# Kernel optimization log

Measured on AMD Instinct MI355X. Metric: run time of the kernel, lower is better.

## Reference

```python
import jax, jax.numpy as jnp
import numpy as np

TOP_K = 2
LN_EPS = 1e-6


def setup_inputs() -> dict:
    key = jax.random.key(0)
    ks = jax.random.split(key, 8)
    B, T, D, FF, E = 4, 512, 1024, 4096, 8
    x = jax.random.normal(ks[0], (B, T, D), dtype=jnp.float32)
    gate_w = jax.random.normal(ks[1], (E, D), dtype=jnp.float32) * (1.0 / np.sqrt(D))
    ln_g = jnp.ones((E, D), dtype=jnp.float32)
    ln_b = jnp.zeros((E, D), dtype=jnp.float32)
    w1 = jax.random.normal(ks[2], (E, FF, D), dtype=jnp.float32) * (1.0 / np.sqrt(D))
    b1 = jnp.zeros((E, FF), dtype=jnp.float32)
    w2 = jax.random.normal(ks[3], (E, D, FF), dtype=jnp.float32) * (1.0 / np.sqrt(FF))
    b2 = jnp.zeros((E, D), dtype=jnp.float32)
    return {"x": x, "gate_w": gate_w, "ln_g": ln_g, "ln_b": ln_b,
            "w1": w1, "b1": b1, "w2": w2, "b2": b2}


def reference(x, gate_w, ln_g, ln_b, w1, b1, w2, b2):
    B, T, D = x.shape
    E = gate_w.shape[0]
    N = B * T
    xf = x.reshape(N, D)

    # ---- Router: linear gate -> softmax -> top-k dispatch mask + aux loss ----
    logits = xf @ gate_w.T                          # [N, E]
    scores = jax.nn.softmax(logits, axis=-1)        # [N, E]
    topk_vals, topk_idx = jax.lax.top_k(scores, TOP_K)
    dispatch = jnp.zeros_like(scores).at[
        jnp.arange(N)[:, None], topk_idx].set(1.0)  # [N, E] 0/1 mask
    load = dispatch.sum(axis=0)                     # [E]
    importance = scores.sum(axis=0)                 # [E]
    aux_loss = (importance * load).sum() * E / (N * N)

    # ---- Experts (PositionwiseFeedForward, kernel_size=1, skip connection) ----
    # Dense-all-experts compute, masked combine: identical math to the
    # per-expert gather/scatter loop in the torch module.
    mu = xf.mean(axis=-1, keepdims=True)
    var = ((xf - mu) ** 2).mean(axis=-1, keepdims=True)
    norm = (xf - mu) / jnp.sqrt(var + LN_EPS)       # [N, D]
    xe = norm[:, None, :] * ln_g[None] + ln_b[None] # [N, E, D] per-expert LN
    h = jax.nn.relu(jnp.einsum('ned,efd->nef', xe, w1) + b1[None])  # [N, E, FF]
    y = jnp.einsum('nef,edf->ned', h, w2) + b2[None] + xf[:, None, :]  # +skip

    comb = scores * dispatch                        # top-k gate weights [N, E]
    out = jnp.einsum('ne,ned->nd', comb, y).reshape(B, T, D)
    return out, aux_loss
```

## Files before the change

### kernel.cpp

```cpp
#include <hip/hip_runtime.h>
#include <hip/hip_bf16.h>

#define N_TOK 2048
#define DMODEL 1024
#define NEXP 8
#define FFDIM 4096
#define NMAX 2048
#define PADROWS 5120
#define TMAX 40

#define BM 128
#define BN 128
#define BK 64
#define KSPL 4

typedef __attribute__((ext_vector_type(8))) short s16x8;
typedef __attribute__((ext_vector_type(4))) float f32x4;

__device__ __forceinline__ float bf2f(ushort u) {
    union { uint i; float f; } x; x.i = ((uint)u) << 16; return x.f;
}
__device__ __forceinline__ ushort f2bf(float f) {
    union { float f; uint i; } x; x.f = f;
    uint r = x.i + 0x7fffu + ((x.i >> 16) & 1u);
    return (ushort)(r >> 16);
}

__device__ __forceinline__ void gl_lds16(const void* g, void* l) {
    __builtin_amdgcn_global_load_lds(
        (const __attribute__((address_space(1))) unsigned int*)g,
        (__attribute__((address_space(3))) unsigned int*)l, 16, 0, 0);
}

__device__ __forceinline__ float block_sum(float v, float* s4) {
    #pragma unroll
    for (int off = 32; off; off >>= 1) v += __shfl_down(v, off);
    __syncthreads();
    if ((threadIdx.x & 63) == 0) s4[threadIdx.x >> 6] = v;
    __syncthreads();
    return s4[0] + s4[1] + s4[2] + s4[3];
}

__global__ __launch_bounds__(256)
void router_kernel(const float* __restrict__ x, const float* __restrict__ gate_w,
                   ushort* __restrict__ norm, float* __restrict__ scores,
                   int* __restrict__ cnt, int* __restrict__ lists,
                   int4* __restrict__ info, float2* __restrict__ gpair) {
    __shared__ float s4[4];
    const int n = blockIdx.x, tid = threadIdx.x;
    const float* xr = x + (size_t)n * DMODEL;
    float4 v = *(const float4*)(xr + tid * 4);

    float tot = block_sum(v.x + v.y + v.z + v.w, s4);
    float mu = tot * (1.0f / DMODEL);
    float d0 = v.x - mu, d1 = v.y - mu, d2 = v.z - mu, d3 = v.w - mu;
    float var = block_sum(d0 * d0 + d1 * d1 + d2 * d2 + d3 * d3, s4) * (1.0f / DMODEL);
    float rstd = rsqrtf(var + 1e-6f);

    ushort nb[4] = { f2bf(d0 * rstd), f2bf(d1 * rstd), f2bf(d2 * rstd), f2bf(d3 * rstd) };
    *(uint2*)(norm + (size_t)n * DMODEL + tid * 4) = *(uint2*)nb;

    float lg[NEXP];
    #pragma unroll
    for (int e = 0; e < NEXP; ++e) {
        float4 g = *(const float4*)(gate_w + (size_t)e * DMODEL + tid * 4);
        lg[e] = v.x * g.x + v.y * g.y + v.z * g.z + v.w * g.w;
    }
    #pragma unroll
    for (int e = 0; e < NEXP; ++e) lg[e] = block_sum(lg[e], s4);

    if (tid == 0) {
        float m = lg[0];
        #pragma unroll
        for (int e = 1; e < NEXP; ++e) m = fmaxf(m, lg[e]);
        float ex[NEXP], Z = 0.f;
        #pragma unroll
        for (int e = 0; e < NEXP; ++e) { ex[e] = expf(lg[e] - m); Z += ex[e]; }
        float inv = 1.0f / Z;
        float sc[NEXP];
        #pragma unroll
        for (int e = 0; e < NEXP; ++e) { sc[e] = ex[e] * inv; scores[n * NEXP + e] = sc[e]; }
        int i1 = 0;
        #pragma unroll
        for (int e = 1; e < NEXP; ++e) if (sc[e] > sc[i1]) i1 = e;
        int i2 = (i1 == 0) ? 1 : 0;
        #pragma unroll
        for (int e = 0; e < NEXP; ++e) if (e != i1 && sc[e] > sc[i2]) i2 = e;
        int s1 = atomicAdd(&cnt[i1], 1);
        lists[i1 * NMAX + s1] = n;
        int s2 = atomicAdd(&cnt[i2], 1);
        lists[i2 * NMAX + s2] = n;
        info[n] = make_int4(i1, s1, i2, s2);
        gpair[n] = make_float2(sc[i1], sc[i2]);
    }
}

__global__ __launch_bounds__(256)
void prep_kernel(const float* __restrict__ scores, const int* __restrict__ cnt,
                 int* __restrict__ offs_pad, int* __restrict__ ntiles,
                 int4* __restrict__ tilemap, float* __restrict__ aux_out) {
    __shared__ float s4[4];
    __shared__ float imp[NEXP];
    float part[NEXP] = {};
    for (int i = threadIdx.x; i < N_TOK; i += 256) {
        #pragma unroll
        for (int e = 0; e < NEXP; ++e) part[e] += scores[i * NEXP + e];
    }
    #pragma unroll
    for (int e = 0; e < NEXP; ++e) {
        float s = block_sum(part[e], s4);
        if (threadIdx.x == 0) imp[e] = s;
    }
    __syncthreads();
    if (threadIdx.x == 0) {
        float aux = 0.f; int pad = 0, idx = 0;
        #pragma unroll
        for (int e = 0; e < NEXP; ++e) {
            aux += imp[e] * (float)cnt[e];
            offs_pad[e] = pad;
            int tiles = (cnt[e] + BM - 1) / BM;
            for (int t = 0; t < tiles; ++t)
                tilemap[idx++] = make_int4(e, pad + t * BM, 0, 0);
            pad += tiles * BM;
        }
        offs_pad[NEXP] = pad;
        ntiles[0] = idx;
        aux_out[0] = aux * (float)NEXP / ((float)N_TOK * (float)N_TOK);
    }
}

__global__ __launch_bounds__(256)
void gather_kernel(const ushort* __restrict__ norm, const float* __restrict__ ln_g,
                   const float* __restrict__ ln_b, const int* __restrict__ offs_pad,
                   const int* __restrict__ cnt, const int* __restrict__ lists,
                   ushort* __restrict__ A1) {
    const int r = blockIdx.x;
    int e = 0;
    #pragma unroll
    for (int k = 1; k < NEXP; ++k) if (r >= offs_pad[k]) e = k;
    const int slot = r - offs_pad[e];
    const int t4 = threadIdx.x * 4;
    if (slot >= cnt[e]) {
        ushort z[4] = {};
        *(uint2*)(A1 + (size_t)r * DMODEL + t4) = *(uint2*)z;
        return;
    }
    const int token = lists[e * NMAX + slot];
    uint2 nbv = *(const uint2*)(norm + (size_t)token * DMODEL + t4);
    ushort ns[4]; *(uint2*)ns = nbv;
    float4 gv = *(const float4*)(ln_g + (size_t)e * DMODEL + t4);
    float4 bv = *(const float4*)(ln_b + (size_t)e * DMODEL + t4);
    ushort ob[4] = { f2bf(bf2f(ns[0]) * gv.x + bv.x), f2bf(bf2f(ns[1]) * gv.y + bv.y),
                     f2bf(bf2f(ns[2]) * gv.z + bv.z), f2bf(bf2f(ns[3]) * gv.w + bv.w) };
    *(uint2*)(A1 + (size_t)r * DMODEL + t4) = *(uint2*)ob;
}

template<int KDIM, int NT, int KSPLT, bool RELU>
__global__ __launch_bounds__(256, 3)
void moe_gemm(const ushort* __restrict__ A, const float* __restrict__ W,
              const float* __restrict__ bias, const int* __restrict__ ntiles,
              const int4* __restrict__ tilemap, ushort* __restrict__ hout,
              float* __restrict__ yout) {
    __shared__ ushort As[BM * BK];
    __shared__ float  Wsf[BN * BK];
    constexpr int NOUT = NT * BN;

    const int q = (int)gridDim.x >> 3;
    const int logical = ((int)blockIdx.x & 7) * q + ((int)blockIdx.x >> 3);
    const int bt = logical % TMAX;
    int g = logical / TMAX;
    if (bt >= ntiles[0]) return;
    const int nt = g % NT;
    const int kb = g / NT;
    const int4 tm = tilemap[bt];
    const int e = tm.x, row0 = tm.y;

    const int tid = threadIdx.x, lane = tid & 63, wave = tid >> 6;
    const int wm = (wave & 1) * 64, wn = (wave >> 1) * 64;
    const int trow = lane >> 3;
    const int scol = ((lane & 7) ^ trow) * 8;

    const ushort* Agb = A + (size_t)row0 * KDIM;
    const float*  Wgb = W + ((size_t)e * NOUT + nt * BN) * KDIM;

    const int wrow  = (lane >> 4);
    const int wchnk = (lane & 15);

    f32x4 acc[4][4] = {};

    auto stageA = [&](int step) {
        #pragma unroll
        for (int i = 0; i < 4; ++i) {
            int c = wave * 4 + i;
            gl_lds16(Agb + (size_t)(c * 8 + trow) * KDIM + step * BK + scol, &As[c * 512]);
        }
    };
    auto stageW = [&](int step) {
        #pragma unroll
        for (int i = 0; i < 8; ++i) {
            int r0 = wave * 32 + i * 4;
            int row = r0 + wrow;
            int chunk = wchnk ^ (row & 7);
            gl_lds16(Wgb + (size_t)row * KDIM + step * BK + chunk * 4, &Wsf[r0 * 64]);
        }
    };
    auto readW = [&](int ni, int kki) -> s16x8 {
        const int row = wn + ni * 16 + (lane & 15);
        const int x = row & 7;
        const int cb = kki * 8 + (lane >> 4) * 2;
        const float4 f0 = *(const float4*)&Wsf[row * 64 + ((cb ^ x) << 2)];
        const float4 f1 = *(const float4*)&Wsf[row * 64 + (((cb + 1) ^ x) << 2)];
        union { s16x8 v; __hip_bfloat162 h2[4]; } u;
        u.h2[0] = __float22bfloat162_rn(make_float2(f0.x, f0.y));
        u.h2[1] = __float22bfloat162_rn(make_float2(f0.z, f0.w));
        u.h2[2] = __float22bfloat162_rn(make_float2(f1.x, f1.y));
        u.h2[3] = __float22bfloat162_rn(make_float2(f1.z, f1.w));
        return u.v;
    };
    auto mfma_phase = [&]() {
        #pragma unroll
        for (int kki = 0; kki < 2; ++kki) {
            const int cx = (kki * 32 + (lane >> 4) * 8) ^ ((lane & 7) << 3);
            s16x8 af[4], bfv[4];
            #pragma unroll
            for (int mi = 0; mi < 4; ++mi)
                af[mi] = *(const s16x8*)&As[(wm + mi * 16 + (lane & 15)) * BK + cx];
            #pragma unroll
            for (int ni = 0; ni < 4; ++ni)
                bfv[ni] = readW(ni, kki);
            #pragma unroll
            for (int mi = 0; mi < 4; ++mi)
                #pragma unroll
                for (int ni = 0; ni < 4; ++ni)
                    acc[mi][ni] = __builtin_amdgcn_mfma_f32_16x16x32_bf16(
                        af[mi], bfv[ni], acc[mi][ni], 0, 0, 0);
        }
    };

    const int KS = KDIM / BK / KSPLT;
    const int kt0 = kb * KS;

    for (int s = 0; s < KS; ++s) {
        stageA(kt0 + s);
        stageW(kt0 + s);
        __syncthreads();
        mfma_phase();
        __syncthreads();
    }

    if (RELU) {
        #pragma unroll
        for (int ni = 0; ni < 4; ++ni) {
            const int nn = nt * BN + wn + ni * 16 + (lane & 15);
            const float bv = bias[(size_t)e * NOUT + nn];
            #pragma unroll
            for (int mi = 0; mi < 4; ++mi)
                #pragma unroll
                for (int r = 0; r < 4; ++r) {
                    const int sl = wm + mi * 16 + ((lane >> 4) << 2) + r;
                    hout[(size_t)(row0 + sl) * NOUT + nn] =
                        f2bf(fmaxf(acc[mi][ni][r] + bv, 0.f));
                }
        }
    } else {
        #pragma unroll
        for (int ni = 0; ni < 4; ++ni) {
            const int nn = nt * BN + wn + ni * 16 + (lane & 15);
            #pragma unroll
            for (int mi = 0; mi < 4; ++mi)
                #pragma unroll
                for (int r = 0; r < 4; ++r) {
                    const int sl = wm + mi * 16 + ((lane >> 4) << 2) + r;
                    yout[((size_t)kb * PADROWS + row0 + sl) * NOUT + nn] = acc[mi][ni][r];
                }
        }
    }
}

__global__ __launch_bounds__(256)
void combine_kernel(const float* __restrict__ ypart, const float* __restrict__ b2,
                    const float* __restrict__ x, const int* __restrict__ offs_pad,
                    const int4* __restrict__ info, const float2* __restrict__ gpair,
                    float* __restrict__ out) {
    const int n = blockIdx.x, d = threadIdx.x * 4;
    const int4 ii = info[n];
    const float2 g = gpair[n];
    const int r1 = offs_pad[ii.x] + ii.y, r2 = offs_pad[ii.z] + ii.w;
    f32x4 y1 = {}, y2 = {};
    #pragma unroll
    for (int kb = 0; kb < KSPL; ++kb) {
        y1 += *(const f32x4*)(ypart + ((size_t)kb * PADROWS + r1) * DMODEL + d);
        y2 += *(const f32x4*)(ypart + ((size_t)kb * PADROWS + r2) * DMODEL + d);
    }
    const f32x4 b21 = *(const f32x4*)(b2 + (size_t)ii.x * DMODEL + d);
    const f32x4 b22 = *(const f32x4*)(b2 + (size_t)ii.z * DMODEL + d);
    const f32x4 xv  = *(const f32x4*)(x + (size_t)n * DMODEL + d);
    f32x4 o = g.x * (y1 + b21 + xv) + g.y * (y2 + b22 + xv);
    *(f32x4*)(out + (size_t)n * DMODEL + d) = o;
}

extern "C" void kernel_launch(void* const* d_in, const int* in_sizes, int n_in,
                              void* d_out, int out_size, void* d_ws, size_t ws_size,
                              hipStream_t stream) {
    const float* x      = (const float*)d_in[0];
    const float* gate_w = (const float*)d_in[1];
    const float* ln_g   = (const float*)d_in[2];
    const float* ln_b   = (const float*)d_in[3];
    const float* w1     = (const float*)d_in[4];
    const float* b1     = (const float*)d_in[5];
    const float* w2     = (const float*)d_in[6];
    const float* b2     = (const float*)d_in[7];
    float* out = (float*)d_out;

    char* w = (char*)d_ws;
    int*    cnt      = (int*)(w + 0);
    int*    offs_pad = (int*)(w + 64);
    int*    ntiles   = (int*)(w + 128);
    int4*   tilemap  = (int4*)(w + 192);
    int*    lists    = (int*)(w + 1024);
    float*  scores   = (float*)(w + 66560);
    int4*   info     = (int4*)(w + 132096);
    float2* gpair    = (float2*)(w + 164864);
    ushort* norm     = (ushort*)(w + 181248);
    ushort* A1       = (ushort*)(w + 4375552);
    ushort* h        = (ushort*)(w + 14861312);
    float*  ypart    = (float*)(w + 56804352);

    hipMemsetAsync(cnt, 0, 64, stream);

    router_kernel<<<N_TOK, 256, 0, stream>>>(x, gate_w, norm, scores, cnt, lists, info, gpair);
    prep_kernel<<<1, 256, 0, stream>>>(scores, cnt, offs_pad, ntiles, tilemap,
                                       out + (size_t)N_TOK * DMODEL);
    gather_kernel<<<PADROWS, 256, 0, stream>>>(norm, ln_g, ln_b, offs_pad, cnt, lists, A1);
    moe_gemm<DMODEL, FFDIM / BN, 1, true><<<TMAX * (FFDIM / BN), 256, 0, stream>>>(
        A1, w1, b1, ntiles, tilemap, h, nullptr);
    moe_gemm<FFDIM, DMODEL / BN, KSPL, false><<<TMAX * (DMODEL / BN) * KSPL, 256, 0, stream>>>(
        h, w2, nullptr, ntiles, tilemap, nullptr, ypart);
    combine_kernel<<<N_TOK, 256, 0, stream>>>(ypart, b2, x, offs_pad, info, gpair, out);
}
```

Measured before the change: 258.3 us.

## Double-buffer GEMM tiles and convert weights to bf16 once before LDS store

The MoE GEMM now double-buffers the A and W shared-memory tiles and prefetches the next K-step while the MFMAs for the current step run, which leaves one barrier per iteration. Weights are loaded into registers as fp32, converted to bf16 once and written to LDS with an XOR swizzle. Before, fp32 was stored in LDS and every wave converted it again when reading. This halves W's LDS footprint and removes the repeated conversions, but it adds register pressure from the prefetch registers, and occupancy drops from 3 to 2 blocks per CU.

```diff
diff --git a/kernel.cpp b/kernel.cpp
--- a/kernel.cpp
+++ b/kernel.cpp
@@ -156,13 +156,13 @@
 }
 
 template<int KDIM, int NT, int KSPLT, bool RELU>
-__global__ __launch_bounds__(256, 3)
+__global__ __launch_bounds__(256, 2)
 void moe_gemm(const ushort* __restrict__ A, const float* __restrict__ W,
               const float* __restrict__ bias, const int* __restrict__ ntiles,
               const int4* __restrict__ tilemap, ushort* __restrict__ hout,
               float* __restrict__ yout) {
-    __shared__ ushort As[BM * BK];
-    __shared__ float  Wsf[BN * BK];
+    __shared__ ushort As[2][BM * BK];
+    __shared__ ushort Ws[2][BN * BK];
     constexpr int NOUT = NT * BN;
 
     const int q = (int)gridDim.x >> 3;
@@ -183,51 +183,49 @@
     const ushort* Agb = A + (size_t)row0 * KDIM;
     const float*  Wgb = W + ((size_t)e * NOUT + nt * BN) * KDIM;
 
-    const int wrow  = (lane >> 4);
-    const int wchnk = (lane & 15);
-
     f32x4 acc[4][4] = {};
-
-    auto stageA = [&](int step) {
+    float4 wr[8];
+
+    auto stageA = [&](int step, int b) {
         #pragma unroll
         for (int i = 0; i < 4; ++i) {
             int c = wave * 4 + i;
-            gl_lds16(Agb + (size_t)(c * 8 + trow) * KDIM + step * BK + scol, &As[c * 512]);
+            gl_lds16(Agb + (size_t)(c * 8 + trow) * KDIM + step * BK + scol, &As[b][c * 512]);
         }
     };
-    auto stageW = [&](int step) {
-        #pragma unroll
-        for (int i = 0; i < 8; ++i) {
-            int r0 = wave * 32 + i * 4;
-            int row = r0 + wrow;
-            int chunk = wchnk ^ (row & 7);
-            gl_lds16(Wgb + (size_t)row * KDIM + step * BK + chunk * 4, &Wsf[r0 * 64]);
+    auto loadWreg = [&](int step) {
+        #pragma unroll
+        for (int i = 0; i < 4; ++i) {
+            int c = tid + 256 * i;
+            const float* p = Wgb + (size_t)(c >> 3) * KDIM + step * BK + (c & 7) * 8;
+            wr[2 * i]     = *(const float4*)p;
+            wr[2 * i + 1] = *(const float4*)(p + 4);
         }
     };
-    auto readW = [&](int ni, int kki) -> s16x8 {
-        const int row = wn + ni * 16 + (lane & 15);
-        const int x = row & 7;
-        const int cb = kki * 8 + (lane >> 4) * 2;
-        const float4 f0 = *(const float4*)&Wsf[row * 64 + ((cb ^ x) << 2)];
-        const float4 f1 = *(const float4*)&Wsf[row * 64 + (((cb + 1) ^ x) << 2)];
-        union { s16x8 v; __hip_bfloat162 h2[4]; } u;
-        u.h2[0] = __float22bfloat162_rn(make_float2(f0.x, f0.y));
-        u.h2[1] = __float22bfloat162_rn(make_float2(f0.z, f0.w));
-        u.h2[2] = __float22bfloat162_rn(make_float2(f1.x, f1.y));
-        u.h2[3] = __float22bfloat162_rn(make_float2(f1.z, f1.w));
-        return u.v;
+    auto cvtWriteW = [&](int b) {
+        #pragma unroll
+        for (int i = 0; i < 4; ++i) {
+            int c = tid + 256 * i;
+            int row = c >> 3, col8 = (c & 7) * 8;
+            union { s16x8 v; __hip_bfloat162 h2[4]; } u;
+            u.h2[0] = __float22bfloat162_rn(make_float2(wr[2 * i].x, wr[2 * i].y));
+            u.h2[1] = __float22bfloat162_rn(make_float2(wr[2 * i].z, wr[2 * i].w));
+            u.h2[2] = __float22bfloat162_rn(make_float2(wr[2 * i + 1].x, wr[2 * i + 1].y));
+            u.h2[3] = __float22bfloat162_rn(make_float2(wr[2 * i + 1].z, wr[2 * i + 1].w));
+            *(s16x8*)&Ws[b][row * BK + (col8 ^ ((row & 7) << 3))] = u.v;
+        }
     };
-    auto mfma_phase = [&]() {
+    auto mfma_phase = [&](int b) {
         #pragma unroll
         for (int kki = 0; kki < 2; ++kki) {
             const int cx = (kki * 32 + (lane >> 4) * 8) ^ ((lane & 7) << 3);
             s16x8 af[4], bfv[4];
             #pragma unroll
             for (int mi = 0; mi < 4; ++mi)
-                af[mi] = *(const s16x8*)&As[(wm + mi * 16 + (lane & 15)) * BK + cx];
+                af[mi] = *(const s16x8*)&As[b][(wm + mi * 16 + (lane & 15)) * BK + cx];
             #pragma unroll
             for (int ni = 0; ni < 4; ++ni)
-                bfv[ni] = readW(ni, kki);
+                bfv[ni] = *(const s16x8*)&Ws[b][(wn + ni * 16 + (lane & 15)) * BK + cx];
             #pragma unroll
             for (int mi = 0; mi < 4; ++mi)
                 #pragma unroll
@@ -240,12 +238,21 @@
     const int KS = KDIM / BK / KSPLT;
     const int kt0 = kb * KS;
 
+    loadWreg(kt0);
+    stageA(kt0, 0);
+    cvtWriteW(0);
+    __syncthreads();
+
+    int buf = 0;
     for (int s = 0; s < KS; ++s) {
-        stageA(kt0 + s);
-        stageW(kt0 + s);
+        if (s + 1 < KS) {
+            stageA(kt0 + s + 1, buf ^ 1);
+            loadWreg(kt0 + s + 1);
+        }
+        mfma_phase(buf);
+        if (s + 1 < KS) cvtWriteW(buf ^ 1);
         __syncthreads();
-        mfma_phase();
-        __syncthreads();
+        buf ^= 1;
     }
 
     if (RELU) {
```

Measured after the change: 309.9 us. 20.0% more time.

## Triple-buffer MoE GEMM LDS tiles with 512-thread blocks and async prefetch

Applied to the files above, without the earlier changes.

Moves the expert GEMM to 8 waves per block, each owning a 64x32 output sub-tile. LDS staging becomes a 3-stage ring buffer, with loads issued three K-steps ahead and partially waited on through vmcnt, so global-to-LDS traffic overlaps the MFMA work. The loop is fully unrolled with a hardcoded 16 steps, which holds for both GEMMs (1024/64 and 4096/64/4). The cost is about 144KB of LDS per block, one block per CU, and a correctness dependence on the hand-tuned waitcnt count.

```diff
diff --git a/kernel.cpp b/kernel.cpp
--- a/kernel.cpp
+++ b/kernel.cpp
@@ -156,13 +156,13 @@
 }
 
 template<int KDIM, int NT, int KSPLT, bool RELU>
-__global__ __launch_bounds__(256, 3)
+__global__ __launch_bounds__(512, 1)
 void moe_gemm(const ushort* __restrict__ A, const float* __restrict__ W,
               const float* __restrict__ bias, const int* __restrict__ ntiles,
               const int4* __restrict__ tilemap, ushort* __restrict__ hout,
               float* __restrict__ yout) {
-    __shared__ ushort As[BM * BK];
-    __shared__ float  Wsf[BN * BK];
+    __shared__ ushort As[3][BM * BK];
+    __shared__ float  Wsf[3][BN * BK];
     constexpr int NOUT = NT * BN;
 
     const int q = (int)gridDim.x >> 3;
@@ -176,40 +176,40 @@
     const int e = tm.x, row0 = tm.y;
 
     const int tid = threadIdx.x, lane = tid & 63, wave = tid >> 6;
-    const int wm = (wave & 1) * 64, wn = (wave >> 1) * 64;
-    const int trow = lane >> 3;
-    const int scol = ((lane & 7) ^ trow) * 8;
+    const int wm = (wave >> 2) * 64;
+    const int wn = (wave & 3) * 32;
 
     const ushort* Agb = A + (size_t)row0 * KDIM;
     const float*  Wgb = W + ((size_t)e * NOUT + nt * BN) * KDIM;
 
-    const int wrow  = (lane >> 4);
-    const int wchnk = (lane & 15);
-
-    f32x4 acc[4][4] = {};
-
-    auto stageA = [&](int step) {
+    f32x4 acc[4][2] = {};
+
+    auto stageA = [&](int step, int b) {
+        #pragma unroll
+        for (int i = 0; i < 2; ++i) {
+            const int c = wave * 128 + i * 64 + lane;
+            const int row = c >> 3;
+            const int scolx = (((c & 7) ^ (row & 7)) * 8);
+            gl_lds16(Agb + (size_t)row * KDIM + step * BK + scolx,
+                     &As[b][(wave * 128 + i * 64) * 8]);
+        }
+    };
+    auto stageW = [&](int step, int b) {
         #pragma unroll
         for (int i = 0; i < 4; ++i) {
-            int c = wave * 4 + i;
-            gl_lds16(Agb + (size_t)(c * 8 + trow) * KDIM + step * BK + scol, &As[c * 512]);
+            const int c = wave * 256 + i * 64 + lane;
+            const int row = c >> 4;
+            const int scol = (c & 15) ^ (row & 7);
+            gl_lds16(Wgb + (size_t)row * KDIM + step * BK + scol * 4,
+                     &Wsf[b][(wave * 256 + i * 64) * 4]);
         }
     };
-    auto stageW = [&](int step) {
-        #pragma unroll
-        for (int i = 0; i < 8; ++i) {
-            int r0 = wave * 32 + i * 4;
-            int row = r0 + wrow;
-            int chunk = wchnk ^ (row & 7);
-            gl_lds16(Wgb + (size_t)row * KDIM + step * BK + chunk * 4, &Wsf[r0 * 64]);
-        }
-    };
-    auto readW = [&](int ni, int kki) -> s16x8 {
+    auto readW = [&](int b, int ni, int kki) -> s16x8 {
         const int row = wn + ni * 16 + (lane & 15);
         const int x = row & 7;
         const int cb = kki * 8 + (lane >> 4) * 2;
-        const float4 f0 = *(const float4*)&Wsf[row * 64 + ((cb ^ x) << 2)];
-        const float4 f1 = *(const float4*)&Wsf[row * 64 + (((cb + 1) ^ x) << 2)];
+        const float4 f0 = *(const float4*)&Wsf[b][row * 64 + ((cb ^ x) << 2)];
+        const float4 f1 = *(const float4*)&Wsf[b][row * 64 + (((cb + 1) ^ x) << 2)];
         union { s16x8 v; __hip_bfloat162 h2[4]; } u;
         u.h2[0] = __float22bfloat162_rn(make_float2(f0.x, f0.y));
         u.h2[1] = __float22bfloat162_rn(make_float2(f0.z, f0.w));
@@ -217,21 +217,21 @@
         u.h2[3] = __float22bfloat162_rn(make_float2(f1.z, f1.w));
         return u.v;
     };
-    auto mfma_phase = [&]() {
+    auto mfma_phase = [&](int b) {
         #pragma unroll
         for (int kki = 0; kki < 2; ++kki) {
             const int cx = (kki * 32 + (lane >> 4) * 8) ^ ((lane & 7) << 3);
-            s16x8 af[4], bfv[4];
+            s16x8 af[4], bfv[2];
             #pragma unroll
             for (int mi = 0; mi < 4; ++mi)
-                af[mi] = *(const s16x8*)&As[(wm + mi * 16 + (lane & 15)) * BK + cx];
-            #pragma unroll
-            for (int ni = 0; ni < 4; ++ni)
-                bfv[ni] = readW(ni, kki);
+                af[mi] = *(const s16x8*)&As[b][(wm + mi * 16 + (lane & 15)) * BK + cx];
+            #pragma unroll
+            for (int ni = 0; ni < 2; ++ni)
+                bfv[ni] = readW(b, ni, kki);
             #pragma unroll
             for (int mi = 0; mi < 4; ++mi)
                 #pragma unroll
-                for (int ni = 0; ni < 4; ++ni)
+                for (int ni = 0; ni < 2; ++ni)
                     acc[mi][ni] = __builtin_amdgcn_mfma_f32_16x16x32_bf16(
                         af[mi], bfv[ni], acc[mi][ni], 0, 0, 0);
         }
@@ -240,17 +240,31 @@
     const int KS = KDIM / BK / KSPLT;
     const int kt0 = kb * KS;
 
-    for (int s = 0; s < KS; ++s) {
-        stageA(kt0 + s);
-        stageW(kt0 + s);
-        __syncthreads();
-        mfma_phase();
-        __syncthreads();
-    }
+    stageA(kt0 + 0, 0); stageW(kt0 + 0, 0);
+    stageA(kt0 + 1, 1); stageW(kt0 + 1, 1);
+    stageA(kt0 + 2, 2); stageW(kt0 + 2, 2);
+    __builtin_amdgcn_sched_barrier(0);
+
+    #pragma unroll
+    for (int s = 0; s < 16; ++s) {
+        asm volatile("s_waitcnt vmcnt(12)" ::: "memory");
+        __builtin_amdgcn_sched_barrier(0);
+        __builtin_amdgcn_s_barrier();
+        __builtin_amdgcn_sched_barrier(0);
+        mfma_phase(s % 3);
+        __builtin_amdgcn_sched_barrier(0);
+        __builtin_amdgcn_s_barrier();
+        __builtin_amdgcn_sched_barrier(0);
+        const int nxt = (s + 3 < 16) ? (kt0 + s + 3) : (kt0 + 15);
+        stageA(nxt, s % 3);
+        stageW(nxt, s % 3);
+        __builtin_amdgcn_sched_barrier(0);
+    }
+    asm volatile("s_waitcnt vmcnt(0)" ::: "memory");
 
     if (RELU) {
         #pragma unroll
-        for (int ni = 0; ni < 4; ++ni) {
+        for (int ni = 0; ni < 2; ++ni) {
             const int nn = nt * BN + wn + ni * 16 + (lane & 15);
             const float bv = bias[(size_t)e * NOUT + nn];
             #pragma unroll
@@ -264,7 +278,7 @@
         }
     } else {
         #pragma unroll
-        for (int ni = 0; ni < 4; ++ni) {
+        for (int ni = 0; ni < 2; ++ni) {
             const int nn = nt * BN + wn + ni * 16 + (lane & 15);
             #pragma unroll
             for (int mi = 0; mi < 4; ++mi)
@@ -332,9 +346,9 @@
     prep_kernel<<<1, 256, 0, stream>>>(scores, cnt, offs_pad, ntiles, tilemap,
                                        out + (size_t)N_TOK * DMODEL);
     gather_kernel<<<PADROWS, 256, 0, stream>>>(norm, ln_g, ln_b, offs_pad, cnt, lists, A1);
-    moe_gemm<DMODEL, FFDIM / BN, 1, true><<<TMAX * (FFDIM / BN), 256, 0, stream>>>(
+    moe_gemm<DMODEL, FFDIM / BN, 1, true><<<TMAX * (FFDIM / BN), 512, 0, stream>>>(
         A1, w1, b1, ntiles, tilemap, h, nullptr);
-    moe_gemm<FFDIM, DMODEL / BN, KSPL, false><<<TMAX * (DMODEL / BN) * KSPL, 256, 0, stream>>>(
+    moe_gemm<FFDIM, DMODEL / BN, KSPL, false><<<TMAX * (DMODEL / BN) * KSPL, 512, 0, stream>>>(
         h, w2, nullptr, ntiles, tilemap, nullptr, ypart);
     combine_kernel<<<N_TOK, 256, 0, stream>>>(ypart, b2, x, offs_pad, info, gpair, out);
 }
```

Result: slower. 354.8 us (+37.4%).
